# Kernel optimization log

Hardware: AMD Instinct MI355X
Metric: run time of the kernel (lower is better)

## Reference

```python
import jax, jax.numpy as jnp
import numpy as np

D = 1024
H = 16
HD = D // H
SCALE = HD ** -0.5


def setup_inputs() -> dict:
    key = jax.random.key(0)
    ks = jax.random.split(key, 5)
    x = jax.random.normal(ks[0], (2, 2048, D), dtype=jnp.float32)
    s = 1.0 / np.sqrt(D)
    W_qkv = jax.random.uniform(ks[1], (D, 3 * D), jnp.float32, -s, s)
    b_qkv = jax.random.uniform(ks[2], (3 * D,), jnp.float32, -s, s)
    W_out = jax.random.uniform(ks[3], (D, D), jnp.float32, -s, s)
    b_out = jax.random.uniform(ks[4], (D,), jnp.float32, -s, s)
    return {"x": x, "W_qkv": W_qkv, "b_qkv": b_qkv, "W_out": W_out, "b_out": b_out}


def reference(x, W_qkv, b_qkv, W_out, b_out):
    B, S, _ = x.shape
    qkv = x @ W_qkv + b_qkv                       # [B,S,3D]
    qkv = qkv.reshape(B, S, 3, H, HD)
    q, k, v = jnp.moveaxis(qkv, 2, 0)             # each [B,S,H,HD]
    # scores: [B,H,S,S]
    scores = jnp.einsum("bshd,bthd->bhst", q, k) * SCALE
    attn = jax.nn.softmax(scores, axis=-1)        # dropout is identity in eval mode
    out = jnp.einsum("bhst,bthd->bshd", attn, v)  # [B,S,H,HD]
    out = out.reshape(B, S, H * HD)
    return out @ W_out + b_out
```

## Files before the change

kernel.cpp:

```cpp
#include <hip/hip_runtime.h>

typedef unsigned short u16;
typedef unsigned int   u32;

using short8 = __attribute__((ext_vector_type(8))) short;
using f32x4  = __attribute__((ext_vector_type(4))) float;
using half4  = __attribute__((ext_vector_type(4))) _Float16;
using half8  = __attribute__((ext_vector_type(8))) _Float16;

#define QSCALE 0.18033688011112042f

__device__ __forceinline__ u16 f2bf(float f) {
  u32 u = __float_as_uint(f);
  return (u16)((u + 0x8000u) >> 16);
}
__device__ __forceinline__ u16 f2h(float f) {
  _Float16 h = (_Float16)f;
  return __builtin_bit_cast(u16, h);
}

__device__ __forceinline__ void gld16(const u16* g, u16* l) {
  __builtin_amdgcn_global_load_lds(
      (const __attribute__((address_space(1))) unsigned int*)g,
      (__attribute__((address_space(3))) unsigned int*)l, 16, 0, 0);
}

__global__ __launch_bounds__(256) void cvt_x(const float* __restrict__ in,
                                             u16* __restrict__ out) {
  int idx = blockIdx.x * 256 + threadIdx.x;
  float4 v = reinterpret_cast<const float4*>(in)[idx];
  ushort4 o;
  o.x = f2bf(v.x); o.y = f2bf(v.y); o.z = f2bf(v.z); o.w = f2bf(v.w);
  reinterpret_cast<ushort4*>(out)[idx] = o;
}

__global__ __launch_bounds__(256) void transpose_w(const float* __restrict__ in,
                                                   u16* __restrict__ out,
                                                   int R, int C) {
  __shared__ u32 s[32][33];
  int c0 = blockIdx.x * 32, r0 = blockIdx.y * 32;
  int j = threadIdx.x & 31, i0 = threadIdx.x >> 5;
#pragma unroll
  for (int p = 0; p < 4; ++p) {
    int i = i0 + p * 8;
    s[i][j] = f2bf(in[(size_t)(r0 + i) * C + c0 + j]);
  }
  __syncthreads();
#pragma unroll
  for (int p = 0; p < 4; ++p) {
    int jj = i0 + p * 8;
    out[(size_t)(c0 + jj) * R + r0 + j] = (u16)s[j][jj];
  }
}

template <int EPI, int MT>
__global__ __launch_bounds__(256, 3) void gemm_bt(
    const u16* __restrict__ A, const u16* __restrict__ Bt,
    const float* __restrict__ bias, float* __restrict__ c_out,
    u16* __restrict__ q_out, u16* __restrict__ k_out, u16* __restrict__ vt_out,
    int M, int N, int K) {
  __shared__ __align__(16) u16 As[32 * MT * 32];
  __shared__ __align__(16) u16 Bs[128 * 32];
  const int tid = threadIdx.x;
  const int lane = tid & 63;
  const int wv = tid >> 6;
  const int l16 = lane & 15, quad = lane >> 4;
  const int wm = wv & 1, wn = wv >> 1;
  const int bx = blockIdx.x, by = blockIdx.y;

  const u16* Ab = A + (size_t)by * (32 * MT) * K;
  const u16* Bb = Bt + (size_t)bx * 128 * K;

  const f32x4 fzero = {0.0f, 0.0f, 0.0f, 0.0f};
  f32x4 acc[MT][4];
#pragma unroll
  for (int i = 0; i < MT; ++i)
#pragma unroll
    for (int j = 0; j < 4; ++j) acc[i][j] = fzero;

  for (int k0 = 0; k0 < K; k0 += 32) {
    __syncthreads();
#pragma unroll
    for (int p = 0; p < MT / 2; ++p) {
      int id = p * 256 + tid;
      int row = id >> 2, blk = id & 3;
      int gc = k0 + ((blk ^ (row & 3)) << 3);
      gld16(Ab + (size_t)row * K + gc, &As[id << 3]);
    }
#pragma unroll
    for (int p = 0; p < 2; ++p) {
      int id = p * 256 + tid;
      int row = id >> 2, blk = id & 3;
      int gc = k0 + ((blk ^ (row & 3)) << 3);
      gld16(Bb + (size_t)row * K + gc, &Bs[id << 3]);
    }
    __syncthreads();
    short8 af[MT], bfr[4];
#pragma unroll
    for (int mi = 0; mi < MT; ++mi) {
      int row = wm * (MT * 16) + mi * 16 + l16;
      af[mi] = *reinterpret_cast<const short8*>(&As[row * 32 + ((quad ^ (row & 3)) << 3)]);
    }
#pragma unroll
    for (int ni = 0; ni < 4; ++ni) {
      int row = wn * 64 + ni * 16 + l16;
      bfr[ni] = *reinterpret_cast<const short8*>(&Bs[row * 32 + ((quad ^ (row & 3)) << 3)]);
    }
#pragma unroll
    for (int mi = 0; mi < MT; ++mi)
#pragma unroll
      for (int ni = 0; ni < 4; ++ni)
        acc[mi][ni] = __builtin_amdgcn_mfma_f32_16x16x32_bf16(af[mi], bfr[ni], acc[mi][ni], 0, 0, 0);
  }

#pragma unroll
  for (int mi = 0; mi < MT; ++mi)
#pragma unroll
    for (int ni = 0; ni < 4; ++ni) {
      int col = bx * 128 + wn * 64 + ni * 16 + l16;
      float bv = bias[col];
      int row0 = by * (32 * MT) + wm * (MT * 16) + mi * 16 + quad * 4;
      if (EPI == 1) {
#pragma unroll
        for (int r = 0; r < 4; ++r)
          c_out[(size_t)(row0 + r) * N + col] = acc[mi][ni][r] + bv;
      } else {
        int which = col >> 10, rem = col & 1023;
        int h = rem >> 6, d = rem & 63;
        int b = row0 >> 11, sq0 = row0 & 2047;
        int bh = (b << 4) + h;
        if (which == 2) {
          ushort4 pk;
          pk.x = f2h(acc[mi][ni][0] + bv);
          pk.y = f2h(acc[mi][ni][1] + bv);
          pk.z = f2h(acc[mi][ni][2] + bv);
          pk.w = f2h(acc[mi][ni][3] + bv);
          size_t off = (size_t)bh * 131072 +
                       (((sq0 >> 2) * 16 + (d & 15)) * 16 + ((d >> 4) << 2));
          *reinterpret_cast<ushort4*>(&vt_out[off]) = pk;
        } else {
          size_t base = (size_t)(bh * 2048 + sq0) * 64 + d;
#pragma unroll
          for (int r = 0; r < 4; ++r) {
            float val = acc[mi][ni][r] + bv;
            if (which == 0) q_out[base + r * 64] = f2bf(val * QSCALE);
            else            k_out[base + r * 64] = f2bf(val);
          }
        }
      }
    }
}

__global__ __launch_bounds__(256, 4) void attn(
    const u16* __restrict__ q_buf, const u16* __restrict__ k_buf,
    const u16* __restrict__ vt_buf, u16* __restrict__ o_buf) {
  __shared__ __align__(16) float red[4][4][256];
  __shared__ float lred[4][16];

  const int tid = threadIdx.x;
  const int lane = tid & 63, w = tid >> 6;
  const int l16 = lane & 15, quad = lane >> 4;
  const int bh = blockIdx.x, q0 = blockIdx.y * 32;

  const u16* qg = q_buf + (size_t)bh * 131072 + q0 * 64;
  const u16* kp = k_buf + (size_t)bh * 131072 + (w * 16 + l16) * 64 + quad * 8;
  const u16* vp = vt_buf + (size_t)bh * 131072 + ((w * 4 + quad) * 16 + l16) * 16;

  short8 qb[2][2];
#pragma unroll
  for (int qi = 0; qi < 2; ++qi)
#pragma unroll
    for (int kk = 0; kk < 2; ++kk)
      qb[qi][kk] = *reinterpret_cast<const short8*>(
          qg + (qi * 16 + l16) * 64 + kk * 32 + quad * 8);

  const f32x4 fzero = {0.0f, 0.0f, 0.0f, 0.0f};
  f32x4 o_acc[2][4];
  float l_acc[2] = {0.f, 0.f};
#pragma unroll
  for (int qi = 0; qi < 2; ++qi)
#pragma unroll
    for (int nd = 0; nd < 4; ++nd) o_acc[qi][nd] = fzero;

  short8 ka[2][2];
  ka[0][0] = *reinterpret_cast<const short8*>(kp);
  ka[0][1] = *reinterpret_cast<const short8*>(kp + 32);

#pragma unroll 2
  for (int i = 0; i < 32; ++i) {
    const int buf = i & 1, nb = buf ^ 1;

    half8 v0 = *reinterpret_cast<const half8*>(vp);
    half8 v1 = *reinterpret_cast<const half8*>(vp + 8);
    vp += 4096;

    if (i + 1 < 32) {
      const u16* kn = kp + (size_t)4096;
      ka[nb][0] = *reinterpret_cast<const short8*>(kn);
      ka[nb][1] = *reinterpret_cast<const short8*>(kn + 32);
      kp = kn;
    }

    short8 k0 = ka[buf][0], k1 = ka[buf][1];
    half4 vb0 = __builtin_shufflevector(v0, v0, 0, 1, 2, 3);
    half4 vb1 = __builtin_shufflevector(v0, v0, 4, 5, 6, 7);
    half4 vb2 = __builtin_shufflevector(v1, v1, 0, 1, 2, 3);
    half4 vb3 = __builtin_shufflevector(v1, v1, 4, 5, 6, 7);

#pragma unroll
    for (int qi = 0; qi < 2; ++qi) {
      f32x4 s = __builtin_amdgcn_mfma_f32_16x16x32_bf16(k0, qb[qi][0], fzero, 0, 0, 0);
      s = __builtin_amdgcn_mfma_f32_16x16x32_bf16(k1, qb[qi][1], s, 0, 0, 0);
      float p0 = __builtin_amdgcn_exp2f(s[0]);
      float p1 = __builtin_amdgcn_exp2f(s[1]);
      float p2 = __builtin_amdgcn_exp2f(s[2]);
      float p3 = __builtin_amdgcn_exp2f(s[3]);
      l_acc[qi] += (p0 + p1) + (p2 + p3);
      half4 pa;
      pa[0] = (_Float16)p0; pa[1] = (_Float16)p1;
      pa[2] = (_Float16)p2; pa[3] = (_Float16)p3;
      o_acc[qi][0] = __builtin_amdgcn_mfma_f32_16x16x16f16(pa, vb0, o_acc[qi][0], 0, 0, 0);
      o_acc[qi][1] = __builtin_amdgcn_mfma_f32_16x16x16f16(pa, vb1, o_acc[qi][1], 0, 0, 0);
      o_acc[qi][2] = __builtin_amdgcn_mfma_f32_16x16x16f16(pa, vb2, o_acc[qi][2], 0, 0, 0);
      o_acc[qi][3] = __builtin_amdgcn_mfma_f32_16x16x16f16(pa, vb3, o_acc[qi][3], 0, 0, 0);
    }
  }

#pragma unroll
  for (int qi = 0; qi < 2; ++qi) {
    l_acc[qi] += __shfl_xor(l_acc[qi], 16, 64);
    l_acc[qi] += __shfl_xor(l_acc[qi], 32, 64);
  }

  const int b = bh >> 4, h = bh & 15;
#pragma unroll
  for (int qi = 0; qi < 2; ++qi) {
#pragma unroll
    for (int nd = 0; nd < 4; ++nd)
      *reinterpret_cast<f32x4*>(&red[w][nd][lane * 4]) = o_acc[qi][nd];
    if (lane < 16) lred[w][lane] = l_acc[qi];
    __syncthreads();
    f32x4 os = fzero, lv = fzero;
#pragma unroll
    for (int wp = 0; wp < 4; ++wp) {
      os += *reinterpret_cast<const f32x4*>(&red[wp][w][lane * 4]);
      lv += *reinterpret_cast<const f32x4*>(&lred[wp][quad * 4]);
    }
#pragma unroll
    for (int r = 0; r < 4; ++r) {
      int sq = q0 + qi * 16 + quad * 4 + r;
      o_buf[(size_t)(b * 2048 + sq) * 1024 + h * 64 + w * 16 + l16] =
          f2bf(os[r] / lv[r]);
    }
    __syncthreads();
  }
}

extern "C" void kernel_launch(void* const* d_in, const int* in_sizes, int n_in,
                              void* d_out, int out_size, void* d_ws, size_t ws_size,
                              hipStream_t stream) {
  (void)in_sizes; (void)n_in; (void)out_size; (void)ws_size;
  const float* x     = (const float*)d_in[0];
  const float* W_qkv = (const float*)d_in[1];
  const float* b_qkv = (const float*)d_in[2];
  const float* W_out = (const float*)d_in[3];
  const float* b_out = (const float*)d_in[4];
  float* out = (float*)d_out;

  char* ws = (char*)d_ws;
  u16* x_bf   = (u16*)(ws);
  u16* wqkv_t = (u16*)(ws + 8388608);
  u16* wout_t = (u16*)(ws + 14680064);
  u16* q_buf  = (u16*)(ws + 16777216);
  u16* k_buf  = (u16*)(ws + 25165824);
  u16* vt_buf = (u16*)(ws + 33554432);
  u16* o_bf   = (u16*)(ws + 41943040);

  cvt_x<<<4096, 256, 0, stream>>>(x, x_bf);
  transpose_w<<<dim3(96, 32), 256, 0, stream>>>(W_qkv, wqkv_t, 1024, 3072);
  transpose_w<<<dim3(32, 32), 256, 0, stream>>>(W_out, wout_t, 1024, 1024);
  gemm_bt<0, 4><<<dim3(24, 32), 256, 0, stream>>>(x_bf, wqkv_t, b_qkv, nullptr,
                                                  q_buf, k_buf, vt_buf, 4096, 3072, 1024);
  attn<<<dim3(32, 64), 256, 0, stream>>>(q_buf, k_buf, vt_buf, o_bf);
  gemm_bt<1, 2><<<dim3(8, 64), 256, 0, stream>>>(o_bf, wout_t, b_out, out,
                                                 nullptr, nullptr, nullptr, 4096, 1024, 1024);
}
```

Before: 220.5 us.

## Stage K/V tiles in LDS shared across waves, each wave owning query rows

The attention kernel previously split each block's keys across four waves, each loading K/V straight from global memory, then reduced partial outputs through LDS. Now each block handles 128 queries, with each wave owning 32 of them. K and V tiles of 64 keys are loaded once per block into LDS with global_load_lds (K rows XOR-swizzled) and shared by all waves, so the cross-wave reduction disappears. This cuts global K/V traffic per query by four and removes the epilogue syncs. In exchange it adds two block barriers per iteration without double buffering, and the grid shrinks to 512 blocks.

```diff
diff --git a/kernel.cpp b/kernel.cpp
--- a/kernel.cpp
+++ b/kernel.cpp
@@ -154,17 +154,17 @@
 __global__ __launch_bounds__(256, 4) void attn(
     const u16* __restrict__ q_buf, const u16* __restrict__ k_buf,
     const u16* __restrict__ vt_buf, u16* __restrict__ o_buf) {
-  __shared__ __align__(16) float red[4][4][256];
-  __shared__ float lred[4][16];
+  __shared__ __align__(16) u16 Ks[64 * 64];
+  __shared__ __align__(16) u16 Vs[4096];
 
   const int tid = threadIdx.x;
   const int lane = tid & 63, w = tid >> 6;
   const int l16 = lane & 15, quad = lane >> 4;
-  const int bh = blockIdx.x, q0 = blockIdx.y * 32;
-
-  const u16* qg = q_buf + (size_t)bh * 131072 + q0 * 64;
-  const u16* kp = k_buf + (size_t)bh * 131072 + (w * 16 + l16) * 64 + quad * 8;
-  const u16* vp = vt_buf + (size_t)bh * 131072 + ((w * 4 + quad) * 16 + l16) * 16;
+  const int bh = blockIdx.x, q0 = blockIdx.y * 128;
+
+  const u16* qg = q_buf + (size_t)bh * 131072 + (q0 + w * 32) * 64;
+  const u16* kg = k_buf + (size_t)bh * 131072;
+  const u16* vg = vt_buf + (size_t)bh * 131072;
 
   short8 qb[2][2];
 #pragma unroll
@@ -182,47 +182,51 @@
 #pragma unroll
     for (int nd = 0; nd < 4; ++nd) o_acc[qi][nd] = fzero;
 
-  short8 ka[2][2];
-  ka[0][0] = *reinterpret_cast<const short8*>(kp);
-  ka[0][1] = *reinterpret_cast<const short8*>(kp + 32);
-
-#pragma unroll 2
   for (int i = 0; i < 32; ++i) {
-    const int buf = i & 1, nb = buf ^ 1;
-
-    half8 v0 = *reinterpret_cast<const half8*>(vp);
-    half8 v1 = *reinterpret_cast<const half8*>(vp + 8);
-    vp += 4096;
-
-    if (i + 1 < 32) {
-      const u16* kn = kp + (size_t)4096;
-      ka[nb][0] = *reinterpret_cast<const short8*>(kn);
-      ka[nb][1] = *reinterpret_cast<const short8*>(kn + 32);
-      kp = kn;
-    }
-
-    short8 k0 = ka[buf][0], k1 = ka[buf][1];
-    half4 vb0 = __builtin_shufflevector(v0, v0, 0, 1, 2, 3);
-    half4 vb1 = __builtin_shufflevector(v0, v0, 4, 5, 6, 7);
-    half4 vb2 = __builtin_shufflevector(v1, v1, 0, 1, 2, 3);
-    half4 vb3 = __builtin_shufflevector(v1, v1, 4, 5, 6, 7);
-
-#pragma unroll
-    for (int qi = 0; qi < 2; ++qi) {
-      f32x4 s = __builtin_amdgcn_mfma_f32_16x16x32_bf16(k0, qb[qi][0], fzero, 0, 0, 0);
-      s = __builtin_amdgcn_mfma_f32_16x16x32_bf16(k1, qb[qi][1], s, 0, 0, 0);
-      float p0 = __builtin_amdgcn_exp2f(s[0]);
-      float p1 = __builtin_amdgcn_exp2f(s[1]);
-      float p2 = __builtin_amdgcn_exp2f(s[2]);
-      float p3 = __builtin_amdgcn_exp2f(s[3]);
-      l_acc[qi] += (p0 + p1) + (p2 + p3);
-      half4 pa;
-      pa[0] = (_Float16)p0; pa[1] = (_Float16)p1;
-      pa[2] = (_Float16)p2; pa[3] = (_Float16)p3;
-      o_acc[qi][0] = __builtin_amdgcn_mfma_f32_16x16x16f16(pa, vb0, o_acc[qi][0], 0, 0, 0);
-      o_acc[qi][1] = __builtin_amdgcn_mfma_f32_16x16x16f16(pa, vb1, o_acc[qi][1], 0, 0, 0);
-      o_acc[qi][2] = __builtin_amdgcn_mfma_f32_16x16x16f16(pa, vb2, o_acc[qi][2], 0, 0, 0);
-      o_acc[qi][3] = __builtin_amdgcn_mfma_f32_16x16x16f16(pa, vb3, o_acc[qi][3], 0, 0, 0);
+    __syncthreads();
+#pragma unroll
+    for (int p = 0; p < 2; ++p) {
+      int id = p * 256 + tid;
+      int krow = id >> 3, kblk = id & 7;
+      gld16(kg + (size_t)krow * 64 + ((kblk ^ (krow & 7)) << 3), &Ks[id << 3]);
+      gld16(vg + (id << 3), &Vs[id << 3]);
+    }
+    kg += 4096;
+    vg += 4096;
+    __syncthreads();
+
+#pragma unroll
+    for (int tsub = 0; tsub < 4; ++tsub) {
+      int rr = tsub * 16 + l16;
+      short8 k0f = *reinterpret_cast<const short8*>(
+          &Ks[rr * 64 + ((quad ^ (rr & 7)) << 3)]);
+      short8 k1f = *reinterpret_cast<const short8*>(
+          &Ks[rr * 64 + (((4 + quad) ^ (rr & 7)) << 3)]);
+      const u16* vbp = &Vs[((tsub * 4 + quad) * 16 + l16) * 16];
+      half8 v0 = *reinterpret_cast<const half8*>(vbp);
+      half8 v1 = *reinterpret_cast<const half8*>(vbp + 8);
+      half4 vb0 = __builtin_shufflevector(v0, v0, 0, 1, 2, 3);
+      half4 vb1 = __builtin_shufflevector(v0, v0, 4, 5, 6, 7);
+      half4 vb2 = __builtin_shufflevector(v1, v1, 0, 1, 2, 3);
+      half4 vb3 = __builtin_shufflevector(v1, v1, 4, 5, 6, 7);
+
+#pragma unroll
+      for (int qi = 0; qi < 2; ++qi) {
+        f32x4 s = __builtin_amdgcn_mfma_f32_16x16x32_bf16(k0f, qb[qi][0], fzero, 0, 0, 0);
+        s = __builtin_amdgcn_mfma_f32_16x16x32_bf16(k1f, qb[qi][1], s, 0, 0, 0);
+        float p0 = __builtin_amdgcn_exp2f(s[0]);
+        float p1 = __builtin_amdgcn_exp2f(s[1]);
+        float p2 = __builtin_amdgcn_exp2f(s[2]);
+        float p3 = __builtin_amdgcn_exp2f(s[3]);
+        l_acc[qi] += (p0 + p1) + (p2 + p3);
+        half4 pa;
+        pa[0] = (_Float16)p0; pa[1] = (_Float16)p1;
+        pa[2] = (_Float16)p2; pa[3] = (_Float16)p3;
+        o_acc[qi][0] = __builtin_amdgcn_mfma_f32_16x16x16f16(pa, vb0, o_acc[qi][0], 0, 0, 0);
+        o_acc[qi][1] = __builtin_amdgcn_mfma_f32_16x16x16f16(pa, vb1, o_acc[qi][1], 0, 0, 0);
+        o_acc[qi][2] = __builtin_amdgcn_mfma_f32_16x16x16f16(pa, vb2, o_acc[qi][2], 0, 0, 0);
+        o_acc[qi][3] = __builtin_amdgcn_mfma_f32_16x16x16f16(pa, vb3, o_acc[qi][3], 0, 0, 0);
+      }
     }
   }
 
@@ -235,24 +239,19 @@
   const int b = bh >> 4, h = bh & 15;
 #pragma unroll
   for (int qi = 0; qi < 2; ++qi) {
-#pragma unroll
-    for (int nd = 0; nd < 4; ++nd)
-      *reinterpret_cast<f32x4*>(&red[w][nd][lane * 4]) = o_acc[qi][nd];
-    if (lane < 16) lred[w][lane] = l_acc[qi];
-    __syncthreads();
-    f32x4 os = fzero, lv = fzero;
-#pragma unroll
-    for (int wp = 0; wp < 4; ++wp) {
-      os += *reinterpret_cast<const f32x4*>(&red[wp][w][lane * 4]);
-      lv += *reinterpret_cast<const f32x4*>(&lred[wp][quad * 4]);
-    }
-#pragma unroll
-    for (int r = 0; r < 4; ++r) {
-      int sq = q0 + qi * 16 + quad * 4 + r;
-      o_buf[(size_t)(b * 2048 + sq) * 1024 + h * 64 + w * 16 + l16] =
-          f2bf(os[r] / lv[r]);
-    }
-    __syncthreads();
+    float lv[4];
+#pragma unroll
+    for (int r = 0; r < 4; ++r)
+      lv[r] = __shfl(l_acc[qi], quad * 4 + r, 64);
+#pragma unroll
+    for (int nd = 0; nd < 4; ++nd) {
+#pragma unroll
+      for (int r = 0; r < 4; ++r) {
+        int sq = q0 + w * 32 + qi * 16 + quad * 4 + r;
+        o_buf[(size_t)(b * 2048 + sq) * 1024 + h * 64 + nd * 16 + l16] =
+            f2bf(o_acc[qi][nd][r] / lv[r]);
+      }
+    }
   }
 }
 
@@ -281,7 +280,7 @@
   transpose_w<<<dim3(32, 32), 256, 0, stream>>>(W_out, wout_t, 1024, 1024);
   gemm_bt<0, 4><<<dim3(24, 32), 256, 0, stream>>>(x_bf, wqkv_t, b_qkv, nullptr,
                                                   q_buf, k_buf, vt_buf, 4096, 3072, 1024);
-  attn<<<dim3(32, 64), 256, 0, stream>>>(q_buf, k_buf, vt_buf, o_bf);
+  attn<<<dim3(32, 16), 256, 0, stream>>>(q_buf, k_buf, vt_buf, o_bf);
   gemm_bt<1, 2><<<dim3(8, 64), 256, 0, stream>>>(o_bf, wout_t, b_out, out,
                                                  nullptr, nullptr, nullptr, 4096, 1024, 1024);
 }
```

New measurement: 192.9 us. 1.14x faster.
